# Kernel tuning notes

Measured on AMD Instinct MI355X. Metric: run time of the kernel, lower is better.

## Reference

```python
import jax, jax.numpy as jnp
import numpy as np

D = 128        # node/time feature dim (n_node_features)
E = 20         # edge feature dim (hard-coded in TGS)
N = 4096       # number of source nodes
K = 10         # neighbors per node (hard-coded n_neighbors=10)
NUM_NODES = 100000
NUM_EDGES = 500000


def setup_inputs() -> dict:
    key = jax.random.key(0)
    ks = jax.random.split(key, 11)
    node_features = jax.random.normal(ks[0], (NUM_NODES, D), jnp.float32)
    edge_features = jax.random.normal(ks[1], (NUM_EDGES, E), jnp.float32)
    source_nodes = jax.random.randint(ks[2], (N,), 0, NUM_NODES)
    timestamps = jax.random.uniform(ks[3], (N,), jnp.float32) * 1000.0
    neighbors1 = jax.random.randint(ks[4], (N, K), 0, NUM_NODES)
    edge_idxs1 = jax.random.randint(ks[5], (N, K), 0, NUM_EDGES)
    edge_times1 = jax.random.uniform(ks[6], (N, K), jnp.float32) * 1000.0
    neighbors2 = jax.random.randint(ks[7], (N * K, K), 0, NUM_NODES)
    edge_idxs2 = jax.random.randint(ks[8], (N * K, K), 0, NUM_EDGES)
    edge_times2 = jax.random.uniform(ks[9], (N * K, K), jnp.float32) * 1000.0
    # TimeEncode params (TGN init: w = 1/10^linspace(0,9,D), b = 0)
    time_w = jnp.asarray(1.0 / 10.0 ** np.linspace(0, 9, D), jnp.float32)
    time_b = jnp.zeros((D,), jnp.float32)
    pk = jax.random.split(ks[10], 4)
    s1 = float(1.0 / np.sqrt(2 * D + E))
    lin1_w = jax.random.uniform(pk[0], (2, 2 * D + E, D), jnp.float32, -s1, s1)
    lin1_b = jax.random.uniform(pk[1], (2, D), jnp.float32, -s1, s1)
    s2 = float(1.0 / np.sqrt(3 * D))
    lin2_w = jax.random.uniform(pk[2], (2, 3 * D, D), jnp.float32, -s2, s2)
    lin2_b = jax.random.uniform(pk[3], (2, D), jnp.float32, -s2, s2)
    return dict(node_features=node_features, edge_features=edge_features,
                source_nodes=source_nodes, timestamps=timestamps,
                neighbors1=neighbors1, edge_idxs1=edge_idxs1, edge_times1=edge_times1,
                neighbors2=neighbors2, edge_idxs2=edge_idxs2, edge_times2=edge_times2,
                time_w=time_w, time_b=time_b,
                lin1_w=lin1_w, lin1_b=lin1_b, lin2_w=lin2_w, lin2_b=lin2_b)


def reference(node_features, edge_features, source_nodes, timestamps,
              neighbors1, edge_idxs1, edge_times1,
              neighbors2, edge_idxs2, edge_times2,
              time_w, time_b, lin1_w, lin1_b, lin2_w, lin2_b):
    def time_enc(t):
        # TGN TimeEncode: cos(t * w + b), broadcast over feature dim
        return jnp.cos(t[..., None] * time_w + time_b)

    def aggregate(layer, src_feat, src_time_emb, nbr_emb, edge_time_emb, edge_feat):
        # GraphSumEmbedding.aggregate
        nf = jnp.concatenate([nbr_emb, edge_time_emb, edge_feat], axis=-1)  # [n, K, 2D+E]
        h = nf @ lin1_w[layer] + lin1_b[layer]                              # [n, K, D]
        nbr_sum = jax.nn.relu(h.sum(axis=1))                                # [n, D]
        sf = jnp.concatenate([src_feat, src_time_emb, nbr_sum], axis=-1)   # [n, 3D]
        return sf @ lin2_w[layer] + lin2_b[layer]                           # [n, D]

    n, k = neighbors1.shape
    ts1 = jnp.repeat(timestamps, k)  # timestamps for the N*K first-hop neighbors

    # recursion level 1 (layer index 0): embed the N*K first-hop neighbors;
    # their neighbors' (level-0) embeddings are raw node features.
    emb1 = aggregate(
        0,
        node_features[neighbors1.reshape(-1)],          # [N*K, D]
        time_enc(jnp.zeros_like(ts1)),                  # [N*K, D]
        node_features[neighbors2],                      # [N*K, K, D]
        time_enc(ts1[:, None] - edge_times2),           # [N*K, K, D]
        edge_features[edge_idxs2])                      # [N*K, K, E]

    # recursion level 2 (layer index 1): embed the N source nodes
    emb2 = aggregate(
        1,
        node_features[source_nodes],                    # [N, D]
        time_enc(jnp.zeros_like(timestamps)),           # [N, D]
        emb1.reshape(n, k, -1),                         # [N, K, D]
        time_enc(timestamps[:, None] - edge_times1),    # [N, K, D]
        edge_features[edge_idxs1])                      # [N, K, E]
    return emb2
```

## Files before the change

### kernel.cpp

```cpp
#include <hip/hip_runtime.h>

#define TGS_D 128
#define TGS_E 20
#define TGS_K 10
#define TGS_F1 276
#define RPB 16

typedef _Float16 f16;
typedef _Float16 f16x8 __attribute__((ext_vector_type(8)));
typedef float    f32x4 __attribute__((ext_vector_type(4)));

__global__ __launch_bounds__(256)
void tgs_nf16(const float* __restrict__ NF, f16* __restrict__ NF16) {
    const int i = (blockIdx.x * 256 + threadIdx.x) * 8;
    const float4 a = *(const float4*)(NF + i);
    const float4 b = *(const float4*)(NF + i + 4);
    *(f16x8*)(NF16 + i) = f16x8{(f16)a.x, (f16)a.y, (f16)a.z, (f16)a.w,
                                (f16)b.x, (f16)b.y, (f16)b.z, (f16)b.w};
}

__global__ __launch_bounds__(128)
void tgs_setup(const float* __restrict__ W1, const float* __restrict__ W2,
               const float* __restrict__ tb, const float* __restrict__ B2,
               f16x8* __restrict__ PW1, f16x8* __restrict__ PW2,
               float* __restrict__ tvec) {
    const int b = blockIdx.x, tid = threadIdx.x;
    if (b < 144) {
        if (tid < 64) {
            const int layer = b / 72, rem = b % 72, ntile = rem / 9, kk = rem % 9;
            const int colg = ntile * 16 + (tid & 15);
            const int kbase = kk * 32 + (tid >> 4) * 8;
            f16x8 v;
            #pragma unroll
            for (int j = 0; j < 8; ++j) {
                const int k = kbase + j;
                v[j] = (k < TGS_F1) ? (f16)W1[(layer * TGS_F1 + k) * TGS_D + colg] : (f16)0.f;
            }
            PW1[b * 64 + tid] = v;
        }
    } else if (b < 272) {
        if (tid < 64) {
            const int bb = b - 144;
            const int layer = bb / 64, rem = bb % 64, ntile = rem / 8, kk = rem % 8;
            const int colg = ntile * 16 + (tid & 15);
            const int kbase = kk * 32 + (tid >> 4) * 8;
            f16x8 v;
            #pragma unroll
            for (int j = 0; j < 8; ++j) {
                const int k = kbase + j;
                const int w2row = (k < TGS_D) ? k : (k + TGS_D);
                v[j] = (f16)W2[(layer * 3 * TGS_D + w2row) * TGS_D + colg];
            }
            PW2[bb * 64 + tid] = v;
        }
    } else {
        const int l = b - 272, d = tid;
        const float* w = W2 + (l * 3 * TGS_D + TGS_D) * TGS_D;
        float acc = B2[l * TGS_D + d];
        for (int j = 0; j < TGS_D; ++j)
            acc = fmaf(__cosf(tb[j]), w[j * TGS_D + d], acc);
        tvec[l * TGS_D + d] = acc;
    }
}

template<int LEVEL>
__global__ __launch_bounds__(64, 2)
void tgs_agg_kernel(
    const f16* __restrict__ NF16, const float* __restrict__ EF,
    const int* __restrict__ src_ids, const float* __restrict__ ts_arr,
    const int* __restrict__ nbr_idx,
    const int* __restrict__ eidx, const float* __restrict__ etime,
    const f16* __restrict__ emb_in,
    const float* __restrict__ tw, const float* __restrict__ tb,
    const f16x8* __restrict__ PW1, const float* __restrict__ B1,
    const f16x8* __restrict__ PW2, const float* __restrict__ tvec,
    void* __restrict__ out_p)
{
    __shared__ f16 s_h[RPB][136];

    const int lane = threadIdx.x;
    const int r    = lane & 15;
    const int hi   = lane >> 4;
    const int base_row = blockIdx.x * RPB;
    const int row  = base_row + r;

    float etv[10];
    #pragma unroll
    for (int p = 0; p < 5; ++p) {
        const float2 t = *(const float2*)(etime + row * TGS_K + p * 2);
        etv[p * 2] = t.x; etv[p * 2 + 1] = t.y;
    }
    const float ts = (LEVEL == 1) ? ts_arr[row / TGS_K] : ts_arr[row];
    const int  sid = src_ids[row];

    f16x8 af[9];

    if (LEVEL == 1) {
        int nb[10];
        #pragma unroll
        for (int p = 0; p < 5; ++p) {
            const int2 t = *(const int2*)(nbr_idx + row * TGS_K + p * 2);
            nb[p * 2] = t.x; nb[p * 2 + 1] = t.y;
        }
        #pragma unroll
        for (int q = 0; q < 4; ++q) {
            f16x8 v[10];
            #pragma unroll
            for (int k = 0; k < TGS_K; ++k)
                v[k] = *(const f16x8*)(NF16 + (size_t)nb[k] * TGS_D + hi * 8 + 32 * q);
            float a[8] = {0.f,0.f,0.f,0.f,0.f,0.f,0.f,0.f};
            #pragma unroll
            for (int k = 0; k < TGS_K; ++k)
                #pragma unroll
                for (int j = 0; j < 8; ++j) a[j] += (float)v[k][j];
            #pragma unroll
            for (int j = 0; j < 8; ++j) af[q][j] = (f16)a[j];
        }
    } else {
        #pragma unroll
        for (int q = 0; q < 4; ++q) {
            f16x8 v[10];
            #pragma unroll
            for (int k = 0; k < TGS_K; ++k)
                v[k] = *(const f16x8*)(emb_in + (size_t)(row * TGS_K + k) * TGS_D + hi * 8 + 32 * q);
            float a[8] = {0.f,0.f,0.f,0.f,0.f,0.f,0.f,0.f};
            #pragma unroll
            for (int k = 0; k < TGS_K; ++k)
                #pragma unroll
                for (int j = 0; j < 8; ++j) a[j] += (float)v[k][j];
            #pragma unroll
            for (int j = 0; j < 8; ++j) af[q][j] = (f16)a[j];
        }
    }

    f16x8 sf[4];
    #pragma unroll
    for (int q = 0; q < 4; ++q)
        sf[q] = *(const f16x8*)(NF16 + (size_t)sid * TGS_D + hi * 8 + 32 * q);

    {
        float a[8] = {0.f,0.f,0.f,0.f,0.f,0.f,0.f,0.f};
        if (hi < 3) {
            int ei[10];
            #pragma unroll
            for (int p = 0; p < 5; ++p) {
                const int2 t = *(const int2*)(eidx + row * TGS_K + p * 2);
                ei[p * 2] = t.x; ei[p * 2 + 1] = t.y;
            }
            if (hi < 2) {
                #pragma unroll
                for (int k = 0; k < TGS_K; ++k) {
                    const float* p = EF + (size_t)ei[k] * TGS_E + hi * 8;
                    const float4 u0 = ((const float4*)p)[0];
                    const float4 u1 = ((const float4*)p)[1];
                    a[0] += u0.x; a[1] += u0.y; a[2] += u0.z; a[3] += u0.w;
                    a[4] += u1.x; a[5] += u1.y; a[6] += u1.z; a[7] += u1.w;
                }
            } else {
                #pragma unroll
                for (int k = 0; k < TGS_K; ++k) {
                    const float4 u0 = *(const float4*)(EF + (size_t)ei[k] * TGS_E + 16);
                    a[0] += u0.x; a[1] += u0.y; a[2] += u0.z; a[3] += u0.w;
                }
            }
        }
        #pragma unroll
        for (int j = 0; j < 8; ++j) af[8][j] = (f16)a[j];
    }

    #pragma unroll
    for (int q = 0; q < 4; ++q) {
        float wv[8], bv[8];
        *(float4*)&wv[0] = *(const float4*)(tw + q * 32 + hi * 8);
        *(float4*)&wv[4] = *(const float4*)(tw + q * 32 + hi * 8 + 4);
        *(float4*)&bv[0] = *(const float4*)(tb + q * 32 + hi * 8);
        *(float4*)&bv[4] = *(const float4*)(tb + q * 32 + hi * 8 + 4);
        float s[8] = {0.f,0.f,0.f,0.f,0.f,0.f,0.f,0.f};
        #pragma unroll
        for (int k = 0; k < TGS_K; ++k) {
            const float dt = ts - etv[k];
            #pragma unroll
            for (int j = 0; j < 8; ++j) {
                const float arg = fmaf(dt, wv[j], bv[j]);
                s[j] += (q < 2) ? __cosf(arg) : fmaf(-0.5f * arg, arg, 1.0f);
            }
        }
        #pragma unroll
        for (int j = 0; j < 8; ++j) af[4 + q][j] = (f16)s[j];
    }

    #pragma unroll
    for (int nt = 0; nt < 8; ++nt) {
        f16x8 bf[9];
        #pragma unroll
        for (int kk = 0; kk < 9; ++kk) bf[kk] = PW1[(nt * 9 + kk) * 64 + lane];
        f32x4 acc = {0.f, 0.f, 0.f, 0.f};
        #pragma unroll
        for (int kk = 0; kk < 9; ++kk)
            acc = __builtin_amdgcn_mfma_f32_16x16x32_f16(af[kk], bf[kk], acc, 0, 0, 0);
        const float bb = 10.f * B1[nt * 16 + r];
        #pragma unroll
        for (int i = 0; i < 4; ++i)
            s_h[hi * 4 + i][nt * 16 + r] = (f16)fmaxf(acc[i] + bb, 0.f);
    }

    f16x8 hf[4];
    #pragma unroll
    for (int q = 0; q < 4; ++q)
        hf[q] = *(const f16x8*)&s_h[r][hi * 8 + 32 * q];

    #pragma unroll
    for (int nt = 0; nt < 8; ++nt) {
        f16x8 bf[8];
        #pragma unroll
        for (int kk = 0; kk < 8; ++kk) bf[kk] = PW2[(nt * 8 + kk) * 64 + lane];
        f32x4 acc = {0.f, 0.f, 0.f, 0.f};
        #pragma unroll
        for (int q = 0; q < 4; ++q)
            acc = __builtin_amdgcn_mfma_f32_16x16x32_f16(sf[q], bf[q], acc, 0, 0, 0);
        #pragma unroll
        for (int q = 0; q < 4; ++q)
            acc = __builtin_amdgcn_mfma_f32_16x16x32_f16(hf[q], bf[4 + q], acc, 0, 0, 0);
        const float tv = tvec[nt * 16 + r];
        if (LEVEL == 2) {
            float* outf = (float*)out_p;
            #pragma unroll
            for (int i = 0; i < 4; ++i)
                outf[(size_t)(base_row + hi * 4 + i) * TGS_D + nt * 16 + r] = acc[i] + tv;
        } else {
            #pragma unroll
            for (int i = 0; i < 4; ++i)
                s_h[hi * 4 + i][nt * 16 + r] = (f16)(acc[i] + tv);
        }
    }
    if (LEVEL == 1) {
        f16* emb_out = (f16*)out_p;
        #pragma unroll
        for (int t = 0; t < 4; ++t) {
            const int m = t * 4 + hi;
            *(f16x8*)(emb_out + (size_t)(base_row + m) * TGS_D + r * 8) =
                *(const f16x8*)&s_h[m][r * 8];
        }
    }
}

extern "C" void kernel_launch(void* const* d_in, const int* in_sizes, int n_in,
                              void* d_out, int out_size, void* d_ws, size_t ws_size,
                              hipStream_t stream) {
    const float* NF   = (const float*)d_in[0];
    const float* EF   = (const float*)d_in[1];
    const int*   SRC  = (const int*)  d_in[2];
    const float* TS   = (const float*)d_in[3];
    const int*   NBR1 = (const int*)  d_in[4];
    const int*   EI1  = (const int*)  d_in[5];
    const float* ET1  = (const float*)d_in[6];
    const int*   NBR2 = (const int*)  d_in[7];
    const int*   EI2  = (const int*)  d_in[8];
    const float* ET2  = (const float*)d_in[9];
    const float* TW   = (const float*)d_in[10];
    const float* TB   = (const float*)d_in[11];
    const float* W1   = (const float*)d_in[12];
    const float* B1   = (const float*)d_in[13];
    const float* W2   = (const float*)d_in[14];
    const float* B2   = (const float*)d_in[15];

    f16*   emb16 = (f16*)d_ws;
    f16*   NF16  = (f16*)((char*)d_ws + 10485760);
    char*  wsb   = (char*)d_ws + 10485760 + 25600000;
    f16x8* PW1   = (f16x8*)wsb;
    f16x8* PW2   = (f16x8*)(wsb + 147456);
    float* tvec  = (float*)(wsb + 147456 + 131072);

    tgs_nf16 <<<6250, 256, 0, stream>>>(NF, NF16);
    tgs_setup<<<274, 128, 0, stream>>>(W1, W2, TB, B2, PW1, PW2, tvec);

    const int n1 = 4096 * TGS_K;
    const int n2 = 4096;

    tgs_agg_kernel<1><<<n1 / RPB, 64, 0, stream>>>(
        NF16, EF, NBR1, TS, NBR2, EI2, ET2, (const f16*)nullptr,
        TW, TB, PW1, B1, PW2, tvec, emb16);

    tgs_agg_kernel<2><<<n2 / RPB, 64, 0, stream>>>(
        NF16, EF, SRC, TS, nullptr, EI1, ET1, emb16,
        TW, TB,
        PW1 + 8 * 9 * 64, B1 + TGS_D,
        PW2 + 8 * 8 * 64, tvec + TGS_D,
        d_out);
}
```

Baseline: 82.64 us.

## Pre-convert edge features to fp16 and pack four waves per block

Adds a pass that converts the full edge-feature table to fp16 in workspace, and the aggregation kernels gather edge features as f16x4 loads, batching all ten loads before summing. The aggregation kernel now runs four independent 16-row waves per 256-thread block with per-wave shared-memory slices, cutting the block count by four. The extra conversion reads 40MB and writes 20MB of edge features every call, while only a small subset is gathered later. This likely costs more than the gather bandwidth it saves.

```diff
diff --git a/kernel.cpp b/kernel.cpp
--- a/kernel.cpp
+++ b/kernel.cpp
@@ -5,8 +5,10 @@
 #define TGS_K 10
 #define TGS_F1 276
 #define RPB 16
+#define WPB 4
 
 typedef _Float16 f16;
+typedef _Float16 f16x4 __attribute__((ext_vector_type(4)));
 typedef _Float16 f16x8 __attribute__((ext_vector_type(8)));
 typedef float    f32x4 __attribute__((ext_vector_type(4)));
 
@@ -17,6 +19,17 @@
     const float4 b = *(const float4*)(NF + i + 4);
     *(f16x8*)(NF16 + i) = f16x8{(f16)a.x, (f16)a.y, (f16)a.z, (f16)a.w,
                                 (f16)b.x, (f16)b.y, (f16)b.z, (f16)b.w};
+}
+
+__global__ __launch_bounds__(256)
+void tgs_ef16(const float* __restrict__ EF, f16* __restrict__ EF16, int n) {
+    const int i = (blockIdx.x * 256 + threadIdx.x) * 8;
+    if (i + 8 <= n) {
+        const float4 a = *(const float4*)(EF + i);
+        const float4 b = *(const float4*)(EF + i + 4);
+        *(f16x8*)(EF16 + i) = f16x8{(f16)a.x, (f16)a.y, (f16)a.z, (f16)a.w,
+                                    (f16)b.x, (f16)b.y, (f16)b.z, (f16)b.w};
+    }
 }
 
 __global__ __launch_bounds__(128)
@@ -64,9 +77,9 @@
 }
 
 template<int LEVEL>
-__global__ __launch_bounds__(64, 2)
+__global__ __launch_bounds__(256, 4)
 void tgs_agg_kernel(
-    const f16* __restrict__ NF16, const float* __restrict__ EF,
+    const f16* __restrict__ NF16, const f16* __restrict__ EF16,
     const int* __restrict__ src_ids, const float* __restrict__ ts_arr,
     const int* __restrict__ nbr_idx,
     const int* __restrict__ eidx, const float* __restrict__ etime,
@@ -76,12 +89,14 @@
     const f16x8* __restrict__ PW2, const float* __restrict__ tvec,
     void* __restrict__ out_p)
 {
-    __shared__ f16 s_h[RPB][136];
-
-    const int lane = threadIdx.x;
+    __shared__ f16 s_h[WPB][RPB][136];
+
+    const int tid  = threadIdx.x;
+    const int lane = tid & 63;
+    const int wid  = tid >> 6;
     const int r    = lane & 15;
     const int hi   = lane >> 4;
-    const int base_row = blockIdx.x * RPB;
+    const int base_row = (blockIdx.x * WPB + wid) * RPB;
     const int row  = base_row + r;
 
     float etv[10];
@@ -148,19 +163,29 @@
                 ei[p * 2] = t.x; ei[p * 2 + 1] = t.y;
             }
             if (hi < 2) {
+                f16x4 v0[10], v1[10];
                 #pragma unroll
                 for (int k = 0; k < TGS_K; ++k) {
-                    const float* p = EF + (size_t)ei[k] * TGS_E + hi * 8;
-                    const float4 u0 = ((const float4*)p)[0];
-                    const float4 u1 = ((const float4*)p)[1];
-                    a[0] += u0.x; a[1] += u0.y; a[2] += u0.z; a[3] += u0.w;
-                    a[4] += u1.x; a[5] += u1.y; a[6] += u1.z; a[7] += u1.w;
+                    const f16* p = EF16 + (size_t)ei[k] * TGS_E + hi * 8;
+                    v0[k] = *(const f16x4*)p;
+                    v1[k] = *(const f16x4*)(p + 4);
+                }
+                #pragma unroll
+                for (int k = 0; k < TGS_K; ++k) {
+                    a[0] += (float)v0[k][0]; a[1] += (float)v0[k][1];
+                    a[2] += (float)v0[k][2]; a[3] += (float)v0[k][3];
+                    a[4] += (float)v1[k][0]; a[5] += (float)v1[k][1];
+                    a[6] += (float)v1[k][2]; a[7] += (float)v1[k][3];
                 }
             } else {
+                f16x4 v0[10];
+                #pragma unroll
+                for (int k = 0; k < TGS_K; ++k)
+                    v0[k] = *(const f16x4*)(EF16 + (size_t)ei[k] * TGS_E + 16);
                 #pragma unroll
                 for (int k = 0; k < TGS_K; ++k) {
-                    const float4 u0 = *(const float4*)(EF + (size_t)ei[k] * TGS_E + 16);
-                    a[0] += u0.x; a[1] += u0.y; a[2] += u0.z; a[3] += u0.w;
+                    a[0] += (float)v0[k][0]; a[1] += (float)v0[k][1];
+                    a[2] += (float)v0[k][2]; a[3] += (float)v0[k][3];
                 }
             }
         }
@@ -201,13 +226,13 @@
         const float bb = 10.f * B1[nt * 16 + r];
         #pragma unroll
         for (int i = 0; i < 4; ++i)
-            s_h[hi * 4 + i][nt * 16 + r] = (f16)fmaxf(acc[i] + bb, 0.f);
+            s_h[wid][hi * 4 + i][nt * 16 + r] = (f16)fmaxf(acc[i] + bb, 0.f);
     }
 
     f16x8 hf[4];
     #pragma unroll
     for (int q = 0; q < 4; ++q)
-        hf[q] = *(const f16x8*)&s_h[r][hi * 8 + 32 * q];
+        hf[q] = *(const f16x8*)&s_h[wid][r][hi * 8 + 32 * q];
 
     #pragma unroll
     for (int nt = 0; nt < 8; ++nt) {
@@ -230,7 +255,7 @@
         } else {
             #pragma unroll
             for (int i = 0; i < 4; ++i)
-                s_h[hi * 4 + i][nt * 16 + r] = (f16)(acc[i] + tv);
+                s_h[wid][hi * 4 + i][nt * 16 + r] = (f16)(acc[i] + tv);
         }
     }
     if (LEVEL == 1) {
@@ -239,7 +264,7 @@
         for (int t = 0; t < 4; ++t) {
             const int m = t * 4 + hi;
             *(f16x8*)(emb_out + (size_t)(base_row + m) * TGS_D + r * 8) =
-                *(const f16x8*)&s_h[m][r * 8];
+                *(const f16x8*)&s_h[wid][m][r * 8];
         }
     }
 }
@@ -266,23 +291,25 @@
 
     f16*   emb16 = (f16*)d_ws;
     f16*   NF16  = (f16*)((char*)d_ws + 10485760);
-    char*  wsb   = (char*)d_ws + 10485760 + 25600000;
+    f16*   EF16  = (f16*)((char*)d_ws + 10485760 + 25600000);
+    char*  wsb   = (char*)d_ws + 10485760 + 25600000 + 20000000;
     f16x8* PW1   = (f16x8*)wsb;
     f16x8* PW2   = (f16x8*)(wsb + 147456);
     float* tvec  = (float*)(wsb + 147456 + 131072);
 
     tgs_nf16 <<<6250, 256, 0, stream>>>(NF, NF16);
+    tgs_ef16 <<<4883, 256, 0, stream>>>(EF, EF16, 500000 * TGS_E);
     tgs_setup<<<274, 128, 0, stream>>>(W1, W2, TB, B2, PW1, PW2, tvec);
 
     const int n1 = 4096 * TGS_K;
     const int n2 = 4096;
 
-    tgs_agg_kernel<1><<<n1 / RPB, 64, 0, stream>>>(
-        NF16, EF, NBR1, TS, NBR2, EI2, ET2, (const f16*)nullptr,
+    tgs_agg_kernel<1><<<n1 / RPB / WPB, 256, 0, stream>>>(
+        NF16, EF16, NBR1, TS, NBR2, EI2, ET2, (const f16*)nullptr,
         TW, TB, PW1, B1, PW2, tvec, emb16);
 
-    tgs_agg_kernel<2><<<n2 / RPB, 64, 0, stream>>>(
-        NF16, EF, SRC, TS, nullptr, EI1, ET1, emb16,
+    tgs_agg_kernel<2><<<n2 / RPB / WPB, 256, 0, stream>>>(
+        NF16, EF16, SRC, TS, nullptr, EI1, ET1, emb16,
         TW, TB,
         PW1 + 8 * 9 * 64, B1 + TGS_D,
         PW2 + 8 * 8 * 64, tvec + TGS_D,
```

Measured after the change: 146.8 us. 1.78x slower.
